# Kernel tuning notes

Measured on AMD Instinct MI355X. Metric: run time of the kernel, lower is better.

Reference implementation:

```python
import jax, jax.numpy as jnp
import numpy as np

B, S, LC, DIM, H, FFN = 1, 3600, 512, 1536, 12, 8960
HD = DIM // H          # 128
GRID = (4, 30, 30)     # f*h*w == S
K_LEN = 9900           # hardcoded k_lens in SelfAttention.forward
EPS = 1e-6

def _rope_axis_angles(n_pos, dim):
    inv = 1.0 / np.power(10000.0, np.arange(0, dim, 2, dtype=np.float64) / dim)
    return np.outer(np.arange(n_pos), inv)

def _build_rope(grid, head_dim):
    c = head_dim // 2                      # 64
    c1, c2 = c - 2 * (c // 3), c // 3      # 22, 21 (Wan 3D rope split)
    f, h, w = grid
    af = _rope_axis_angles(f, 2 * c1)
    ah = _rope_axis_angles(h, 2 * c2)
    aw = _rope_axis_angles(w, 2 * c2)
    ang = np.concatenate([
        np.broadcast_to(af[:, None, None, :], (f, h, w, c1)),
        np.broadcast_to(ah[None, :, None, :], (f, h, w, c2)),
        np.broadcast_to(aw[None, None, :, :], (f, h, w, c2)),
    ], axis=-1).reshape(f * h * w, c)
    return np.cos(ang).astype(np.float32), np.sin(ang).astype(np.float32)

def setup_inputs():
    key = jax.random.key(0)
    ks = iter(jax.random.split(key, 40))
    cos, sin = _build_rope(GRID, HD)
    inp = {
        'x': jax.random.normal(next(ks), (B, S, DIM), dtype=jnp.float32),
        'context': jax.random.normal(next(ks), (B, LC, DIM), dtype=jnp.float32),
        't_mod': 0.1 * jax.random.normal(next(ks), (B, 6, DIM), dtype=jnp.float32),
        'rope_cos': jnp.asarray(cos), 'rope_sin': jnp.asarray(sin),
        'modulation': jax.random.normal(next(ks), (1, 6, DIM), dtype=jnp.float32) / DIM ** 0.5,
    }
    for p in ('sa', 'ca'):
        for w in ('q', 'k', 'v', 'o'):
            inp[p + '_' + w + 'w'] = 0.02 * jax.random.normal(next(ks), (DIM, DIM), dtype=jnp.float32)
            inp[p + '_' + w + 'b'] = jnp.zeros((DIM,), jnp.float32)
        inp[p + '_nq'] = jnp.ones((DIM,), jnp.float32)
        inp[p + '_nk'] = jnp.ones((DIM,), jnp.float32)
    inp['n3_w'] = jnp.ones((DIM,), jnp.float32)
    inp['n3_b'] = jnp.zeros((DIM,), jnp.float32)
    inp['ffn_w1'] = 0.02 * jax.random.normal(next(ks), (DIM, FFN), dtype=jnp.float32)
    inp['ffn_b1'] = jnp.zeros((FFN,), jnp.float32)
    inp['ffn_w2'] = 0.02 * jax.random.normal(next(ks), (FFN, DIM), dtype=jnp.float32)
    inp['ffn_b2'] = jnp.zeros((DIM,), jnp.float32)
    return inp

def _rms(x, w):
    x32 = x.astype(jnp.float32)
    n = x32 * jax.lax.rsqrt(jnp.mean(x32 * x32, axis=-1, keepdims=True) + EPS)
    return n.astype(x.dtype) * w

def _ln(x, w=None, b=None):
    mu = jnp.mean(x, axis=-1, keepdims=True)
    var = jnp.mean(jnp.square(x - mu), axis=-1, keepdims=True)
    y = (x - mu) * jax.lax.rsqrt(var + EPS)
    return y if w is None else y * w + b

def _rope(x, cos, sin):
    b, s, h, d = x.shape
    x2 = x.reshape(b, s, h, d // 2, 2)
    xe, xo = x2[..., 0], x2[..., 1]
    c, sn = cos[None, :, None, :], sin[None, :, None, :]
    return jnp.stack([xe * c - xo * sn, xe * sn + xo * c], axis=-1).reshape(b, s, h, d)

def _attn(q, k, v, k_len=None):
    # q,k,v: [B,S,H,D]
    scores = jnp.einsum('bqhd,bkhd->bhqk', q, k) * (q.shape[-1] ** -0.5)
    if k_len is not None:
        mask = jnp.arange(k.shape[1]) < k_len
        scores = jnp.where(mask[None, None, None, :], scores, jnp.finfo(scores.dtype).min)
    return jnp.einsum('bhqk,bkhd->bqhd', jax.nn.softmax(scores, axis=-1), v)

def reference(x, context, t_mod, rope_cos, rope_sin, modulation,
              sa_qw, sa_qb, sa_kw, sa_kb, sa_vw, sa_vb, sa_ow, sa_ob, sa_nq, sa_nk,
              ca_qw, ca_qb, ca_kw, ca_kb, ca_vw, ca_vb, ca_ow, ca_ob, ca_nq, ca_nk,
              n3_w, n3_b, ffn_w1, ffn_b1, ffn_w2, ffn_b2):
    mod = modulation + t_mod                      # [B,6,DIM]
    sh_msa, sc_msa, g_msa, sh_mlp, sc_mlp, g_mlp = [mod[:, i:i + 1] for i in range(6)]
    b = x.shape[0]
    # --- self-attention with AdaLN modulate + 3D RoPE + k_lens mask ---
    h = _ln(x) * (1 + sc_msa) + sh_msa
    q = _rms(h @ sa_qw + sa_qb, sa_nq).reshape(b, -1, H, HD)
    k = _rms(h @ sa_kw + sa_kb, sa_nk).reshape(b, -1, H, HD)
    v = (h @ sa_vw + sa_vb).reshape(b, -1, H, HD)
    a = _attn(_rope(q, rope_cos, rope_sin), _rope(k, rope_cos, rope_sin), v, k_len=K_LEN)
    x = x + g_msa * (a.reshape(b, -1, DIM) @ sa_ow + sa_ob)
    # --- cross-attention ---
    hc = _ln(x, n3_w, n3_b)
    q = _rms(hc @ ca_qw + ca_qb, ca_nq).reshape(b, -1, H, HD)
    k = _rms(context @ ca_kw + ca_kb, ca_nk).reshape(b, -1, H, HD)
    v = (context @ ca_vw + ca_vb).reshape(b, -1, H, HD)
    x = x + (_attn(q, k, v).reshape(b, -1, DIM) @ ca_ow + ca_ob)
    # --- gated FFN with AdaLN modulate ---
    h = _ln(x) * (1 + sc_mlp) + sh_mlp
    h = jax.nn.gelu(h @ ffn_w1 + ffn_b1, approximate=True) @ ffn_w2 + ffn_b2
    return x + g_mlp * h
```

## Files before the change

### kernel.cpp

```cpp
#include <hip/hip_runtime.h>
#include <cstdint>

#define S_LEN 3600
#define DMODEL 1536
#define LCTX 512
#define NH 12
#define HDIM 128
#define FFND 8960
#define SPAD_SELF 3648

typedef short v8s __attribute__((ext_vector_type(8)));
typedef float v4f __attribute__((ext_vector_type(4)));
typedef unsigned short u16b;
typedef unsigned int u32b;

#define AS1 __attribute__((address_space(1)))
#define AS3 __attribute__((address_space(3)))

__device__ __forceinline__ void gl_lds16(const void* g, void* l){
  __builtin_amdgcn_global_load_lds((AS1 const void*)g, (AS3 void*)l, 16, 0, 0);
}

__device__ __forceinline__ u16b f2b(float f){
  union { float f; u32b i; } x; x.f = f;
  u32b r = x.i + 0x7fffu + ((x.i >> 16) & 1u);
  return (u16b)(r >> 16);
}

__device__ __forceinline__ u32b cvtpk(float a, float b){
  u32b r;
  asm("v_cvt_pk_bf16_f32 %0, %1, %2" : "=v"(r) : "v"(a), "v"(b));
  return r;
}

__device__ __forceinline__ int swz4(int row){ return (row ^ (row >> 2)) & 3; }

__device__ __forceinline__ int xcd_swz(int orig, int nwg){
  int q8 = nwg >> 3, r8 = nwg & 7;
  int xcd = orig & 7, idx = orig >> 3;
  return (xcd < r8 ? xcd * (q8 + 1) : r8 * (q8 + 1) + (xcd - r8) * q8) + idx;
}

__global__ void add_vec(const float* __restrict__ a, const float* __restrict__ b,
                        float* __restrict__ o, int n){
  int i = blockIdx.x * 256 + threadIdx.x;
  if (i < n) o[i] = a[i] + b[i];
}

__global__ void f2b_kernel(const float* __restrict__ in, u16b* __restrict__ out, int n){
  int i = blockIdx.x * 256 + threadIdx.x;
  if (i < n) out[i] = f2b(in[i]);
}

struct WJob { const float* W; u16b* WT; int K; int N; int t0; };
struct WJobs { WJob j[10]; };

__global__ __launch_bounds__(256) void wconv(WJobs jobs){
  __shared__ float tile[32][33];
  int b = blockIdx.x;
  int ji = 0;
  #pragma unroll
  for (int i = 0; i < 10; ++i) if (b >= jobs.j[i].t0) ji = i;
  WJob jb = jobs.j[ji];
  int rel = b - jb.t0;
  int ntn = jb.N / 32;
  int k0 = (rel / ntn) * 32, n0 = (rel % ntn) * 32;
  int tx = threadIdx.x & 31, ty = threadIdx.x >> 5;
  #pragma unroll
  for (int r = ty; r < 32; r += 8) tile[r][tx] = jb.W[(size_t)(k0 + r) * jb.N + n0 + tx];
  __syncthreads();
  #pragma unroll
  for (int r = ty; r < 32; r += 8) jb.WT[(size_t)(n0 + r) * jb.K + k0 + tx] = f2b(tile[tx][r]);
}

__global__ __launch_bounds__(256) void vtrans(const u16b* __restrict__ V,
                                              u16b* __restrict__ Vt,
                                              int S, int Spad){
  __shared__ u16b t[32][136];
  int h = blockIdx.y, kb = blockIdx.x * 32, tid = threadIdx.x;
  int row = tid >> 3, ch = tid & 7;
  int key = kb + row;
  if (key < S){
    float4 a = *(const float4*)(V + (size_t)key * DMODEL + h * HDIM + ch * 16);
    float4 b = *(const float4*)(V + (size_t)key * DMODEL + h * HDIM + ch * 16 + 8);
    *(float4*)&t[row][ch * 16] = a;
    *(float4*)&t[row][ch * 16 + 8] = b;
  } else {
    float4 z = {0.f, 0.f, 0.f, 0.f};
    *(float4*)&t[row][ch * 16] = z;
    *(float4*)&t[row][ch * 16 + 8] = z;
  }
  __syncthreads();
  int hd = tid >> 1, kc = (tid & 1) * 16;
  u16b* dst = Vt + ((size_t)h * HDIM + hd) * Spad + kb + kc;
  #pragma unroll
  for (int e = 0; e < 16; e += 2){
    u32b pk = ((u32b)t[kc + e][hd]) | (((u32b)t[kc + e + 1][hd]) << 16);
    *(u32b*)(dst + e) = pk;
  }
}

__global__ __launch_bounds__(256) void ln_mod(const float* __restrict__ X,
                                              const float* __restrict__ gamma,
                                              const float* __restrict__ beta,
                                              float gadd, u16b* __restrict__ out){
  int row = blockIdx.x;
  const float* xr = X + (size_t)row * DMODEL;
  int tid = threadIdx.x;
  float v[6]; float s1 = 0.f, s2 = 0.f;
  #pragma unroll
  for (int j = 0; j < 6; ++j){ v[j] = xr[tid + j * 256]; s1 += v[j]; s2 += v[j] * v[j]; }
  #pragma unroll
  for (int o = 1; o < 64; o <<= 1){ s1 += __shfl_xor(s1, o); s2 += __shfl_xor(s2, o); }
  __shared__ float red[8];
  int wid = tid >> 6, lane = tid & 63;
  if (!lane){ red[wid * 2] = s1; red[wid * 2 + 1] = s2; }
  __syncthreads();
  s1 = red[0] + red[2] + red[4] + red[6];
  s2 = red[1] + red[3] + red[5] + red[7];
  float mu = s1 / DMODEL;
  float var = s2 / DMODEL - mu * mu;
  float rstd = rsqrtf(var + 1e-6f);
  #pragma unroll
  for (int j = 0; j < 6; ++j){
    int c = tid + j * 256;
    float g = gamma[c] + gadd;
    float b = beta[c];
    out[(size_t)row * DMODEL + c] = f2b((v[j] - mu) * rstd * g + b);
  }
}

__global__ __launch_bounds__(256) void rms_rope(const float* __restrict__ X,
                                                const float* __restrict__ w,
                                                const float* __restrict__ cosT,
                                                const float* __restrict__ sinT,
                                                float qmul,
                                                u16b* __restrict__ out){
  int row = blockIdx.x;
  const float* xr = X + (size_t)row * DMODEL;
  int tid = threadIdx.x;
  float2 v[3]; float ss = 0.f;
  #pragma unroll
  for (int j = 0; j < 3; ++j){
    v[j] = *(const float2*)(xr + 2 * (tid + j * 256));
    ss += v[j].x * v[j].x + v[j].y * v[j].y;
  }
  #pragma unroll
  for (int o = 1; o < 64; o <<= 1) ss += __shfl_xor(ss, o);
  __shared__ float red[4];
  int wid = tid >> 6, lane = tid & 63;
  if (!lane) red[wid] = ss;
  __syncthreads();
  ss = red[0] + red[1] + red[2] + red[3];
  float rstd = rsqrtf(ss / DMODEL + 1e-6f);
  #pragma unroll
  for (int j = 0; j < 3; ++j){
    int p = tid + j * 256;
    float xe = v[j].x * rstd * w[2 * p];
    float xo = v[j].y * rstd * w[2 * p + 1];
    float oe, oo;
    if (cosT){
      int d = p & 63;
      float c = cosT[row * 64 + d], sn = sinT[row * 64 + d];
      oe = xe * c - xo * sn; oo = xe * sn + xo * c;
    } else { oe = xe; oo = xo; }
    oe *= qmul; oo *= qmul;
    u32b packed = ((u32b)f2b(oe)) | (((u32b)f2b(oo)) << 16);
    *(u32b*)(out + (size_t)row * DMODEL + 2 * p) = packed;
  }
}

struct Seg { const float* bias; float* outF; u16b* outB; };
struct Segs { Seg s[3]; };

template<int EPI>
__global__ __launch_bounds__(256, 2) void gemm_bt(
    const u16b* __restrict__ A, const u16b* __restrict__ BT,
    const float* __restrict__ bias, float* __restrict__ outF,
    float* __restrict__ outF2, u16b* __restrict__ outB,
    int M, int N, int K, int kLen)
{
  __shared__ char Ls[3][16384];
  const int tid = threadIdx.x, lane = tid & 63, wid = tid >> 6;
  const int nwg = gridDim.x * gridDim.y;
  const int swz = xcd_swz(blockIdx.x + gridDim.x * blockIdx.y, nwg);
  const int bm = (swz % gridDim.x) * 128, bn = (swz / gridDim.x) * 128;
  const int kbase = blockIdx.z * kLen;
  const int wm = (wid >> 1) * 64, wn = (wid & 1) * 64;
  v4f acc[4][4] = {};

  const u16b* pA[2]; const u16b* pB[2];
  #pragma unroll
  for (int c = 0; c < 2; ++c){
    int row = c * 64 + (tid >> 2);
    int col = (tid & 3) ^ swz4(row);
    pA[c] = A + (size_t)min(bm + row, M - 1) * K + kbase + col * 8;
    pB[c] = BT + (size_t)(bn + row) * K + kbase + col * 8;
  }
  auto stage = [&](int b){
    char* Lb = Ls[b];
    #pragma unroll
    for (int c = 0; c < 2; ++c){
      gl_lds16(pA[c], Lb + (c * 256 + tid) * 16);
      gl_lds16(pB[c], Lb + 8192 + (c * 256 + tid) * 16);
      pA[c] += 32; pB[c] += 32;
    }
  };

  const int chk = lane >> 4, qr = lane & 15;
  int offA[4], offB[4];
  #pragma unroll
  for (int f = 0; f < 4; ++f){
    int ra = wm + f * 16 + qr;
    offA[f] = ra * 64 + ((chk ^ swz4(ra)) * 16);
    int rb = wn + f * 16 + qr;
    offB[f] = 8192 + rb * 64 + ((chk ^ swz4(rb)) * 16);
  }

  const int nt = kLen / 32;
  stage(0); stage(1);
  int s = 0, sp = 2;
  for (int t = 0; t < nt; ++t){
    if (t + 1 < nt) asm volatile("s_waitcnt vmcnt(4)" ::: "memory");
    else            asm volatile("s_waitcnt vmcnt(0)" ::: "memory");
    __builtin_amdgcn_s_barrier();
    if (t + 2 < nt) stage(sp);
    char* Lb = Ls[s];
    v8s af[4], bfr[4];
    #pragma unroll
    for (int f = 0; f < 4; ++f){
      af[f] = *(const v8s*)(Lb + offA[f]);
      bfr[f] = *(const v8s*)(Lb + offB[f]);
    }
    __builtin_amdgcn_s_setprio(1);
    #pragma unroll
    for (int i = 0; i < 4; ++i)
      #pragma unroll
      for (int j = 0; j < 4; ++j)
        acc[i][j] = __builtin_amdgcn_mfma_f32_16x16x32_bf16(af[i], bfr[j], acc[i][j], 0, 0, 0);
    __builtin_amdgcn_s_setprio(0);
    s = (s == 2) ? 0 : s + 1;
    sp = (sp == 2) ? 0 : sp + 1;
  }
  const int rr = lane >> 4;
  float* op6 = (EPI == 6) ? (blockIdx.z ? outF2 : outF) : outF;
  #pragma unroll
  for (int i = 0; i < 4; ++i){
    #pragma unroll
    for (int j = 0; j < 4; ++j){
      int n = bn + wn + j * 16 + qr;
      float bv = (EPI == 3) ? bias[n] : 0.f;
      #pragma unroll
      for (int r = 0; r < 4; ++r){
        int m = bm + wm + i * 16 + rr * 4 + r;
        if (m < M){
          float val = acc[i][j][r] + bv;
          size_t idx = (size_t)m * N + n;
          if (EPI == 3){
            float t3 = val * val * val;
            float g = val / (1.f + __expf(-1.5957691216057308f * (val + 0.044715f * t3)));
            outB[idx] = f2b(g);
          } else if (EPI == 5){
            outF[(size_t)blockIdx.z * M * N + idx] = val;
          } else {
            op6[idx] = val;
          }
        }
      }
    }
  }
}

__global__ __launch_bounds__(256, 2) void gemm_seg(
    const u16b* __restrict__ A, const u16b* __restrict__ BT,
    Segs segs, int M, int N, int K)
{
  __shared__ char Ls[3][16384];
  const int tid = threadIdx.x, lane = tid & 63, wid = tid >> 6;
  const int nwg = gridDim.x * gridDim.y;
  const int swz = xcd_swz(blockIdx.x + gridDim.x * blockIdx.y, nwg);
  const int bm = (swz % gridDim.x) * 128, bn = (swz / gridDim.x) * 128;
  const int wm = (wid >> 1) * 64, wn = (wid & 1) * 64;
  v4f acc[4][4] = {};

  const u16b* pA[2]; const u16b* pB[2];
  #pragma unroll
  for (int c = 0; c < 2; ++c){
    int row = c * 64 + (tid >> 2);
    int col = (tid & 3) ^ swz4(row);
    pA[c] = A + (size_t)min(bm + row, M - 1) * K + col * 8;
    pB[c] = BT + (size_t)(bn + row) * K + col * 8;
  }
  auto stage = [&](int b){
    char* Lb = Ls[b];
    #pragma unroll
    for (int c = 0; c < 2; ++c){
      gl_lds16(pA[c], Lb + (c * 256 + tid) * 16);
      gl_lds16(pB[c], Lb + 8192 + (c * 256 + tid) * 16);
      pA[c] += 32; pB[c] += 32;
    }
  };

  const int chk = lane >> 4, qr = lane & 15;
  int offA[4], offB[4];
  #pragma unroll
  for (int f = 0; f < 4; ++f){
    int ra = wm + f * 16 + qr;
    offA[f] = ra * 64 + ((chk ^ swz4(ra)) * 16);
    int rb = wn + f * 16 + qr;
    offB[f] = 8192 + rb * 64 + ((chk ^ swz4(rb)) * 16);
  }

  const int nt = K / 32;
  stage(0); stage(1);
  int s = 0, sp = 2;
  for (int t = 0; t < nt; ++t){
    if (t + 1 < nt) asm volatile("s_waitcnt vmcnt(4)" ::: "memory");
    else            asm volatile("s_waitcnt vmcnt(0)" ::: "memory");
    __builtin_amdgcn_s_barrier();
    if (t + 2 < nt) stage(sp);
    char* Lb = Ls[s];
    v8s af[4], bfr[4];
    #pragma unroll
    for (int f = 0; f < 4; ++f){
      af[f] = *(const v8s*)(Lb + offA[f]);
      bfr[f] = *(const v8s*)(Lb + offB[f]);
    }
    __builtin_amdgcn_s_setprio(1);
    #pragma unroll
    for (int i = 0; i < 4; ++i)
      #pragma unroll
      for (int j = 0; j < 4; ++j)
        acc[i][j] = __builtin_amdgcn_mfma_f32_16x16x32_bf16(af[i], bfr[j], acc[i][j], 0, 0, 0);
    __builtin_amdgcn_s_setprio(0);
    s = (s == 2) ? 0 : s + 1;
    sp = (sp == 2) ? 0 : sp + 1;
  }
  const int seg = bn / 1536;
  const Seg sg = segs.s[seg];
  const int rr = lane >> 4;
  #pragma unroll
  for (int i = 0; i < 4; ++i){
    #pragma unroll
    for (int j = 0; j < 4; ++j){
      int nloc = bn - seg * 1536 + wn + j * 16 + qr;
      float bv = sg.bias[nloc];
      #pragma unroll
      for (int r = 0; r < 4; ++r){
        int m = bm + wm + i * 16 + rr * 4 + r;
        if (m < M){
          float val = acc[i][j][r] + bv;
          size_t idx = (size_t)m * 1536 + nloc;
          if (sg.outB) sg.outB[idx] = f2b(val);
          else sg.outF[idx] = val;
        }
      }
    }
  }
}

__global__ __launch_bounds__(256) void red2(const float* __restrict__ p0,
                                            const float* __restrict__ p1,
                                            const float* __restrict__ res,
                                            const float* __restrict__ gate,
                                            const float* __restrict__ bias,
                                            float* __restrict__ out, int total){
  int i4 = blockIdx.x * 256 + threadIdx.x;
  if (i4 * 4 >= total) return;
  int base = i4 * 4, n = base % DMODEL;
  float4 a = *(const float4*)(p0 + base);
  float4 b = *(const float4*)(p1 + base);
  float4 bv = *(const float4*)(bias + n);
  float gx = 1.f, gy = 1.f, gz = 1.f, gw = 1.f;
  if (gate){ float4 g = *(const float4*)(gate + n); gx = g.x; gy = g.y; gz = g.z; gw = g.w; }
  float rx = 0.f, ry = 0.f, rz = 0.f, rw = 0.f;
  if (res){ float4 r = *(const float4*)(res + base); rx = r.x; ry = r.y; rz = r.z; rw = r.w; }
  float4 o;
  o.x = rx + gx * (a.x + b.x + bv.x);
  o.y = ry + gy * (a.y + b.y + bv.y);
  o.z = rz + gz * (a.z + b.z + bv.z);
  o.w = rw + gw * (a.w + b.w + bv.w);
  *(float4*)(out + base) = o;
}

__global__ __launch_bounds__(256) void ffn2_reduce(const float* __restrict__ part,
                                                   const float* __restrict__ res,
                                                   const float* __restrict__ bias,
                                                   const float* __restrict__ gate,
                                                   float* __restrict__ out, int total){
  int i4 = blockIdx.x * 256 + threadIdx.x;
  if (i4 * 4 >= total) return;
  int base = i4 * 4;
  int n = base % DMODEL;
  float4 p0 = *(const float4*)(part + base);
  float4 p1 = *(const float4*)(part + (size_t)total + base);
  float4 p2 = *(const float4*)(part + 2 * (size_t)total + base);
  float4 p3 = *(const float4*)(part + 3 * (size_t)total + base);
  float4 rs = *(const float4*)(res + base);
  float4 bv = *(const float4*)(bias + n);
  float4 gv = *(const float4*)(gate + n);
  float4 o;
  o.x = rs.x + gv.x * (p0.x + p1.x + p2.x + p3.x + bv.x);
  o.y = rs.y + gv.y * (p0.y + p1.y + p2.y + p3.y + bv.y);
  o.z = rs.z + gv.z * (p0.z + p1.z + p2.z + p3.z + bv.z);
  o.w = rs.w + gv.w * (p0.w + p1.w + p2.w + p3.w + bv.w);
  *(float4*)(out + base) = o;
}

__global__ __launch_bounds__(256) void merge_o(const float* __restrict__ op0,
                                               const float* __restrict__ op1,
                                               const float2* __restrict__ ml,
                                               u16b* __restrict__ outO, int Sq){
  int i4 = blockIdx.x * 256 + threadIdx.x;
  const int perRow = DMODEL / 4;
  if (i4 >= Sq * perRow) return;
  int row = i4 / perRow, c4 = (i4 % perRow) * 4;
  int h = c4 >> 7;
  float2 ml0 = ml[h * Sq + row];
  float2 ml1 = ml[NH * Sq + h * Sq + row];
  float M = fmaxf(ml0.x, ml1.x);
  float w0 = exp2f(ml0.x - M), w1 = exp2f(ml1.x - M);
  float inv = 1.f / (ml0.y * w0 + ml1.y * w1);
  float4 a = *(const float4*)(op0 + (size_t)row * DMODEL + c4);
  float4 b = *(const float4*)(op1 + (size_t)row * DMODEL + c4);
  u32b lo = ((u32b)f2b((a.x * w0 + b.x * w1) * inv)) | (((u32b)f2b((a.y * w0 + b.y * w1) * inv)) << 16);
  u32b hi = ((u32b)f2b((a.z * w0 + b.z * w1) * inv)) | (((u32b)f2b((a.w * w0 + b.w * w1) * inv)) << 16);
  uint2 w2; w2.x = lo; w2.y = hi;
  *(uint2*)(outO + (size_t)row * DMODEL + c4) = w2;
}

__global__ __launch_bounds__(256, 4) void flash_attn(
    const u16b* __restrict__ Q, const u16b* __restrict__ Kp,
    const u16b* __restrict__ Vt, u16b* __restrict__ O,
    float* __restrict__ op0, float* __restrict__ op1,
    float2* __restrict__ mlbuf,
    int Sq, int Sk, int ksplit, int Spad)
{
  __shared__ char KV[32768];
  __shared__ char Pall[8192];
  const int tid = threadIdx.x, lane = tid & 63, wid = tid >> 6;
  const int h = blockIdx.y;
  const int z = blockIdx.z;
  const int kbeg = z * ksplit;
  const int kend = min(kbeg + ksplit, Sk);
  const int q0 = blockIdx.x * 64 + wid * 16;
  const int qq = lane & 15, cc = lane >> 4;
  char* Kb = KV; char* Vb = KV + 16384;
  char* Pb = Pall + wid * 2048;

  v8s qf[4];
  {
    int qrow = min(q0 + qq, Sq - 1);
    const u16b* qp = Q + (size_t)qrow * DMODEL + h * HDIM + cc * 8;
    #pragma unroll
    for (int ks = 0; ks < 4; ++ks) qf[ks] = *(const v8s*)(qp + ks * 32);
  }

  auto stage = [&](int kb0){
    #pragma unroll
    for (int c = 0; c < 4; ++c){
      int seg = wid * 4 + c;
      int g = seg * 64 + lane;
      int krow = g >> 4, kcol = (g & 15) ^ (krow & 7);
      gl_lds16(Kp + (size_t)min(kb0 + krow, Sk - 1) * DMODEL + h * HDIM + kcol * 8,
               Kb + seg * 1024);
      int vrow = g >> 3, vcol = (g & 7) ^ (vrow & 7);
      gl_lds16(Vt + ((size_t)h * HDIM + vrow) * Spad + kb0 + vcol * 8,
               Vb + seg * 1024);
    }
  };

  float mrun = -1e30f, lrun = 0.f;
  v4f oacc[8] = {};
  const int nt = (kend - kbeg + 63) >> 6;

  for (int t = 0; t < nt; ++t){
    int kb0 = kbeg + (t << 6);
    stage(kb0);
    __syncthreads();
    v4f sc[4];
    __builtin_amdgcn_s_setprio(1);
    #pragma unroll
    for (int sub = 0; sub < 4; ++sub){
      v4f sa = {0.f, 0.f, 0.f, 0.f};
      int row = sub * 16 + qq;
      #pragma unroll
      for (int ks = 0; ks < 4; ++ks){
        v8s kf = *(const v8s*)(Kb + row * 256 + (((ks * 4 + cc) ^ (row & 7)) * 16));
        sa = __builtin_amdgcn_mfma_f32_16x16x32_bf16(kf, qf[ks], sa, 0, 0, 0);
      }
      sc[sub] = sa;
    }
    __builtin_amdgcn_s_setprio(0);
    if (kb0 + 64 > kend){
      #pragma unroll
      for (int sub = 0; sub < 4; ++sub)
        #pragma unroll
        for (int r = 0; r < 4; ++r)
          if (kb0 + sub * 16 + cc * 4 + r >= kend) sc[sub][r] = -1e30f;
    }
    float m01 = fmaxf(fmaxf(sc[0][0], sc[0][1]), fmaxf(sc[0][2], sc[0][3]));
    float m23 = fmaxf(fmaxf(sc[1][0], sc[1][1]), fmaxf(sc[1][2], sc[1][3]));
    float m45 = fmaxf(fmaxf(sc[2][0], sc[2][1]), fmaxf(sc[2][2], sc[2][3]));
    float m67 = fmaxf(fmaxf(sc[3][0], sc[3][1]), fmaxf(sc[3][2], sc[3][3]));
    float pmax = fmaxf(fmaxf(m01, m23), fmaxf(m45, m67));
    pmax = fmaxf(pmax, __shfl_xor(pmax, 16));
    pmax = fmaxf(pmax, __shfl_xor(pmax, 32));
    if (!__all(pmax <= mrun + 11.54f)){
      float mnew = fmaxf(mrun, pmax);
      float alpha = exp2f(mrun - mnew);
      mrun = mnew;
      float alr[4];
      #pragma unroll
      for (int r = 0; r < 4; ++r) alr[r] = __shfl(alpha, cc * 4 + r);
      #pragma unroll
      for (int f = 0; f < 8; ++f)
        #pragma unroll
        for (int r = 0; r < 4; ++r) oacc[f][r] *= alr[r];
      lrun *= alpha;
    }
    float csum = 0.f;
    #pragma unroll
    for (int sub = 0; sub < 4; ++sub){
      float s0 = 0.f, s1 = 0.f;
      #pragma unroll
      for (int r = 0; r < 4; r += 2){
        float p0 = exp2f(sc[sub][r] - mrun);
        float p1 = exp2f(sc[sub][r + 1] - mrun);
        sc[sub][r] = p0; sc[sub][r + 1] = p1;
        s0 += p0; s1 += p1;
      }
      csum += s0 + s1;
    }
    csum += __shfl_xor(csum, 16);
    csum += __shfl_xor(csum, 32);
    lrun += csum;
    #pragma unroll
    for (int sub = 0; sub < 4; ++sub){
      uint2 w2;
      w2.x = cvtpk(sc[sub][0], sc[sub][1]);
      w2.y = cvtpk(sc[sub][2], sc[sub][3]);
      int gI = sub * 2 + (cc >> 1);
      *(uint2*)(Pb + qq * 128 + ((gI ^ (qq & 7)) * 16) + (cc & 1) * 8) = w2;
    }
    v8s pf0 = *(const v8s*)(Pb + qq * 128 + (((cc) ^ (qq & 7)) * 16));
    v8s pf1 = *(const v8s*)(Pb + qq * 128 + (((4 + cc) ^ (qq & 7)) * 16));
    __builtin_amdgcn_s_setprio(1);
    #pragma unroll
    for (int hdb = 0; hdb < 8; ++hdb){
      int row = hdb * 16 + qq;
      v8s vf0 = *(const v8s*)(Vb + row * 128 + (((cc) ^ (row & 7)) * 16));
      v8s vf1 = *(const v8s*)(Vb + row * 128 + (((4 + cc) ^ (row & 7)) * 16));
      oacc[hdb] = __builtin_amdgcn_mfma_f32_16x16x32_bf16(pf0, vf0, oacc[hdb], 0, 0, 0);
      oacc[hdb] = __builtin_amdgcn_mfma_f32_16x16x32_bf16(pf1, vf1, oacc[hdb], 0, 0, 0);
    }
    __builtin_amdgcn_s_setprio(0);
    __syncthreads();
  }

  if (mlbuf){
    float* op = z ? op1 : op0;
    #pragma unroll
    for (int hdb = 0; hdb < 8; ++hdb)
      #pragma unroll
      for (int r = 0; r < 4; ++r){
        int qrow = q0 + cc * 4 + r;
        if (qrow < Sq)
          op[(size_t)qrow * DMODEL + h * HDIM + hdb * 16 + qq] = oacc[hdb][r];
      }
    if (cc == 0 && q0 + qq < Sq)
      mlbuf[(size_t)z * NH * Sq + (size_t)h * Sq + q0 + qq] = make_float2(mrun, lrun);
  } else {
    float linv = 1.f / lrun;
    float lr[4];
    #pragma unroll
    for (int r = 0; r < 4; ++r) lr[r] = __shfl(linv, cc * 4 + r);
    #pragma unroll
    for (int hdb = 0; hdb < 8; ++hdb)
      #pragma unroll
      for (int r = 0; r < 4; ++r){
        int qrow = q0 + cc * 4 + r;
        if (qrow < Sq)
          O[(size_t)qrow * DMODEL + h * HDIM + hdb * 16 + qq] = f2b(oacc[hdb][r] * lr[r]);
      }
  }
}

extern "C" void kernel_launch(void* const* d_in, const int* in_sizes, int n_in,
                              void* d_out, int out_size, void* d_ws, size_t ws_size,
                              hipStream_t stream){
  (void)in_sizes; (void)n_in; (void)out_size; (void)ws_size;
  const float* x     = (const float*)d_in[0];
  const float* ctx   = (const float*)d_in[1];
  const float* t_mod = (const float*)d_in[2];
  const float* ropec = (const float*)d_in[3];
  const float* ropes = (const float*)d_in[4];
  const float* modu  = (const float*)d_in[5];
  const float* sa_qw = (const float*)d_in[6];  const float* sa_qb = (const float*)d_in[7];
  const float* sa_kw = (const float*)d_in[8];  const float* sa_kb = (const float*)d_in[9];
  const float* sa_vw = (const float*)d_in[10]; const float* sa_vb = (const float*)d_in[11];
  const float* sa_ow = (const float*)d_in[12]; const float* sa_ob = (const float*)d_in[13];
  const float* sa_nq = (const float*)d_in[14]; const float* sa_nk = (const float*)d_in[15];
  const float* ca_qw = (const float*)d_in[16]; const float* ca_qb = (const float*)d_in[17];
  const float* ca_kw = (const float*)d_in[18]; const float* ca_kb = (const float*)d_in[19];
  const float* ca_vw = (const float*)d_in[20]; const float* ca_vb = (const float*)d_in[21];
  const float* ca_ow = (const float*)d_in[22]; const float* ca_ob = (const float*)d_in[23];
  const float* ca_nq = (const float*)d_in[24]; const float* ca_nk = (const float*)d_in[25];
  const float* n3w   = (const float*)d_in[26]; const float* n3b   = (const float*)d_in[27];
  const float* fw1   = (const float*)d_in[28]; const float* fb1   = (const float*)d_in[29];
  const float* fw2   = (const float*)d_in[30]; const float* fb2   = (const float*)d_in[31];
  float* out = (float*)d_out;

  const float QSCALE = 0.08838834764831845f * 1.4426950408889634f;

  char* wsp = (char*)d_ws;
  size_t off = 0;
  auto alloc = [&](size_t b){ void* p = wsp + off; off += (b + 255) & ~(size_t)255; return p; };
  const size_t WW = (size_t)DMODEL * DMODEL * 2;
  float* modc = (float*)alloc(6 * DMODEL * 4);
  u16b* w1T   = (u16b*)alloc((size_t)FFND * DMODEL * 2);
  u16b* w2T   = (u16b*)alloc((size_t)DMODEL * FFND * 2);
  u16b* h_bf  = (u16b*)alloc((size_t)S_LEN * DMODEL * 2);
  float* pre0 = (float*)alloc((size_t)S_LEN * DMODEL * 4);
  size_t region0 = off;
  u16b* sa_qkvT = (u16b*)alloc(3 * WW);
  u16b* sa_owT  = (u16b*)alloc(WW);
  u16b* ca_qwT  = (u16b*)alloc(WW);
  u16b* ca_kvT  = (u16b*)alloc(2 * WW);
  u16b* ca_owT  = (u16b*)alloc(WW);
  float* x2    = (float*)alloc((size_t)S_LEN * DMODEL * 4);
  float* pre2  = (float*)alloc((size_t)LCTX * DMODEL * 4);
  u16b* qb     = (u16b*)alloc((size_t)S_LEN * DMODEL * 2);
  u16b* kb     = (u16b*)alloc((size_t)S_LEN * DMODEL * 2);
  u16b* vb     = (u16b*)alloc((size_t)S_LEN * DMODEL * 2);
  u16b* ab     = (u16b*)alloc((size_t)S_LEN * DMODEL * 2);
  u16b* ctxb   = (u16b*)alloc((size_t)LCTX * DMODEL * 2);
  u16b* k2b    = (u16b*)alloc((size_t)LCTX * DMODEL * 2);
  u16b* v2b    = (u16b*)alloc((size_t)LCTX * DMODEL * 2);
  u16b* vts    = (u16b*)alloc((size_t)NH * HDIM * SPAD_SELF * 2);
  u16b* vtc    = (u16b*)alloc((size_t)NH * HDIM * LCTX * 2);
  u16b* fmid = (u16b*)(wsp + region0);
  float* fpart = (float*)(wsp + region0 + (size_t)S_LEN * FFND * 2);

  add_vec<<<36, 256, 0, stream>>>(modu, t_mod, modc, 6 * DMODEL);

  WJobs jobs; int t = 0;
  auto addjob = [&](int i, const float* w_, u16b* wt, int K, int N){
    jobs.j[i].W = w_; jobs.j[i].WT = wt; jobs.j[i].K = K; jobs.j[i].N = N; jobs.j[i].t0 = t;
    t += (K / 32) * (N / 32);
  };
  addjob(0, sa_qw, sa_qkvT, DMODEL, DMODEL);
  addjob(1, sa_kw, sa_qkvT + (size_t)DMODEL * DMODEL, DMODEL, DMODEL);
  addjob(2, sa_vw, sa_qkvT + (size_t)2 * DMODEL * DMODEL, DMODEL, DMODEL);
  addjob(3, sa_ow, sa_owT, DMODEL, DMODEL);
  addjob(4, ca_qw, ca_qwT, DMODEL, DMODEL);
  addjob(5, ca_kw, ca_kvT, DMODEL, DMODEL);
  addjob(6, ca_vw, ca_kvT + (size_t)DMODEL * DMODEL, DMODEL, DMODEL);
  addjob(7, ca_ow, ca_owT, DMODEL, DMODEL);
  addjob(8, fw1, w1T, DMODEL, FFND);
  addjob(9, fw2, w2T, FFND, DMODEL);
  wconv<<<t, 256, 0, stream>>>(jobs);

  f2b_kernel<<<(LCTX * DMODEL) / 256, 256, 0, stream>>>(ctx, ctxb, LCTX * DMODEL);

  const int RED_G = (S_LEN * DMODEL / 4 + 255) / 256;

  ln_mod<<<S_LEN, 256, 0, stream>>>(x, modc + DMODEL, modc, 1.f, h_bf);
  {
    Segs sg;
    sg.s[0] = { sa_qb, pre0, nullptr };
    sg.s[1] = { sa_kb, x2,   nullptr };
    sg.s[2] = { sa_vb, nullptr, vb   };
    gemm_seg<<<dim3(29, 36), 256, 0, stream>>>(h_bf, sa_qkvT, sg, S_LEN, 3 * DMODEL, DMODEL);
  }
  rms_rope<<<S_LEN, 256, 0, stream>>>(pre0, sa_nq, ropec, ropes, QSCALE, qb);
  rms_rope<<<S_LEN, 256, 0, stream>>>(x2, sa_nk, ropec, ropes, 1.f, kb);
  vtrans<<<dim3(SPAD_SELF / 32, 12), 256, 0, stream>>>(vb, vts, S_LEN, SPAD_SELF);
  flash_attn<<<dim3(57, 12, 2), 256, 0, stream>>>(qb, kb, vts, ab,
      (float*)pre0, (float*)x2, (float2*)vb, S_LEN, S_LEN, 1856, SPAD_SELF);
  merge_o<<<RED_G, 256, 0, stream>>>(
      (const float*)pre0, (const float*)x2, (const float2*)vb, ab, S_LEN);
  gemm_bt<6><<<dim3(29, 12, 2), 256, 0, stream>>>(ab, sa_owT, nullptr,
      (float*)pre0, (float*)qb, nullptr, S_LEN, DMODEL, DMODEL, 768);
  red2<<<RED_G, 256, 0, stream>>>((const float*)pre0, (const float*)qb,
      x, modc + 2 * DMODEL, sa_ob, x2, S_LEN * DMODEL);

  ln_mod<<<S_LEN, 256, 0, stream>>>(x2, n3w, n3b, 0.f, h_bf);
  gemm_bt<6><<<dim3(29, 12, 2), 256, 0, stream>>>(h_bf, ca_qwT, nullptr,
      (float*)qb, (float*)vb, nullptr, S_LEN, DMODEL, DMODEL, 768);
  red2<<<RED_G, 256, 0, stream>>>((const float*)qb, (const float*)vb,
      nullptr, nullptr, ca_qb, pre0, S_LEN * DMODEL);
  {
    Segs sg;
    sg.s[0] = { ca_kb, pre2, nullptr };
    sg.s[1] = { ca_vb, nullptr, v2b  };
    sg.s[2] = { ca_vb, nullptr, v2b  };
    gemm_seg<<<dim3(4, 24), 256, 0, stream>>>(ctxb, ca_kvT, sg, LCTX, 2 * DMODEL, DMODEL);
  }
  rms_rope<<<S_LEN, 256, 0, stream>>>(pre0, ca_nq, nullptr, nullptr, QSCALE, qb);
  rms_rope<<<LCTX, 256, 0, stream>>>(pre2, ca_nk, nullptr, nullptr, 1.f, k2b);
  vtrans<<<dim3(16, 12), 256, 0, stream>>>(v2b, vtc, LCTX, LCTX);
  flash_attn<<<dim3(57, 12, 2), 256, 0, stream>>>(qb, k2b, vtc, ab,
      (float*)pre0, (float*)kb, (float2*)vts, S_LEN, LCTX, 256, LCTX);
  merge_o<<<RED_G, 256, 0, stream>>>(
      (const float*)pre0, (const float*)kb, (const float2*)vts, ab, S_LEN);
  gemm_bt<6><<<dim3(29, 12, 2), 256, 0, stream>>>(ab, ca_owT, nullptr,
      (float*)qb, (float*)sa_qkvT, nullptr, S_LEN, DMODEL, DMODEL, 768);
  red2<<<RED_G, 256, 0, stream>>>((const float*)qb, (const float*)sa_qkvT,
      x2, nullptr, ca_ob, pre0, S_LEN * DMODEL);

  ln_mod<<<S_LEN, 256, 0, stream>>>(pre0, modc + 4 * DMODEL, modc + 3 * DMODEL, 1.f, h_bf);
  gemm_bt<3><<<dim3(29, 70), 256, 0, stream>>>(h_bf, w1T, fb1,
      nullptr, nullptr, fmid, S_LEN, FFND, DMODEL, DMODEL);
  gemm_bt<5><<<dim3(29, 12, 4), 256, 0, stream>>>(fmid, w2T, nullptr,
      fpart, nullptr, nullptr, S_LEN, DMODEL, FFND, FFND / 4);
  ffn2_reduce<<<RED_G, 256, 0, stream>>>(fpart, pre0, fb2, modc + 5 * DMODEL, out, S_LEN * DMODEL);
}
```

Before: 949.2 us.

## Fuse residual reduce with layernorm, widen flash-attn blocks, halve FFN2 split-K

Adds a red2_ln kernel that sums the split-K partials, bias, gate and residual, then applies layernorm in one pass. This replaces two separate red2+ln_mod launches and removes an extra read of the fp32 residual stream. Flash attention now uses 512-thread blocks covering 128 query rows, so each staged K/V tile is shared by twice as many queries; this raises LDS use per block and changes the occupancy hint. FFN2 split-K drops from 4 to 2, which halves partial-buffer traffic but leaves fewer blocks for the GEMM.

```diff
diff --git a/kernel.cpp b/kernel.cpp
--- a/kernel.cpp
+++ b/kernel.cpp
@@ -124,9 +124,44 @@
   #pragma unroll
   for (int j = 0; j < 6; ++j){
     int c = tid + j * 256;
-    float g = gamma[c] + gadd;
-    float b = beta[c];
-    out[(size_t)row * DMODEL + c] = f2b((v[j] - mu) * rstd * g + b);
+    out[(size_t)row * DMODEL + c] = f2b((v[j] - mu) * rstd * (gamma[c] + gadd) + beta[c]);
+  }
+}
+
+__global__ __launch_bounds__(256) void red2_ln(
+    const float* __restrict__ p0, const float* __restrict__ p1,
+    const float* __restrict__ res, const float* __restrict__ gate,
+    const float* __restrict__ bias,
+    const float* __restrict__ gamma, const float* __restrict__ beta, float gadd,
+    float* __restrict__ yOut, u16b* __restrict__ hOut)
+{
+  int row = blockIdx.x, tid = threadIdx.x;
+  size_t base = (size_t)row * DMODEL;
+  float y[6]; float s1 = 0.f, s2 = 0.f;
+  #pragma unroll
+  for (int j = 0; j < 6; ++j){
+    int c = tid + j * 256;
+    float v = p0[base + c] + p1[base + c] + bias[c];
+    if (gate) v *= gate[c];
+    v += res[base + c];
+    y[j] = v; s1 += v; s2 += v * v;
+  }
+  #pragma unroll
+  for (int o = 1; o < 64; o <<= 1){ s1 += __shfl_xor(s1, o); s2 += __shfl_xor(s2, o); }
+  __shared__ float red[8];
+  int wid = tid >> 6, lane = tid & 63;
+  if (!lane){ red[wid * 2] = s1; red[wid * 2 + 1] = s2; }
+  __syncthreads();
+  s1 = red[0] + red[2] + red[4] + red[6];
+  s2 = red[1] + red[3] + red[5] + red[7];
+  float mu = s1 / DMODEL;
+  float var = s2 / DMODEL - mu * mu;
+  float rstd = rsqrtf(var + 1e-6f);
+  #pragma unroll
+  for (int j = 0; j < 6; ++j){
+    int c = tid + j * 256;
+    yOut[base + c] = y[j];
+    hOut[base + c] = f2b((y[j] - mu) * rstd * (gamma[c] + gadd) + beta[c]);
   }
 }
 
@@ -383,30 +418,6 @@
   *(float4*)(out + base) = o;
 }
 
-__global__ __launch_bounds__(256) void ffn2_reduce(const float* __restrict__ part,
-                                                   const float* __restrict__ res,
-                                                   const float* __restrict__ bias,
-                                                   const float* __restrict__ gate,
-                                                   float* __restrict__ out, int total){
-  int i4 = blockIdx.x * 256 + threadIdx.x;
-  if (i4 * 4 >= total) return;
-  int base = i4 * 4;
-  int n = base % DMODEL;
-  float4 p0 = *(const float4*)(part + base);
-  float4 p1 = *(const float4*)(part + (size_t)total + base);
-  float4 p2 = *(const float4*)(part + 2 * (size_t)total + base);
-  float4 p3 = *(const float4*)(part + 3 * (size_t)total + base);
-  float4 rs = *(const float4*)(res + base);
-  float4 bv = *(const float4*)(bias + n);
-  float4 gv = *(const float4*)(gate + n);
-  float4 o;
-  o.x = rs.x + gv.x * (p0.x + p1.x + p2.x + p3.x + bv.x);
-  o.y = rs.y + gv.y * (p0.y + p1.y + p2.y + p3.y + bv.y);
-  o.z = rs.z + gv.z * (p0.z + p1.z + p2.z + p3.z + bv.z);
-  o.w = rs.w + gv.w * (p0.w + p1.w + p2.w + p3.w + bv.w);
-  *(float4*)(out + base) = o;
-}
-
 __global__ __launch_bounds__(256) void merge_o(const float* __restrict__ op0,
                                                const float* __restrict__ op1,
                                                const float2* __restrict__ ml,
@@ -429,7 +440,7 @@
   *(uint2*)(outO + (size_t)row * DMODEL + c4) = w2;
 }
 
-__global__ __launch_bounds__(256, 4) void flash_attn(
+__global__ __launch_bounds__(512, 6) void flash_attn(
     const u16b* __restrict__ Q, const u16b* __restrict__ Kp,
     const u16b* __restrict__ Vt, u16b* __restrict__ O,
     float* __restrict__ op0, float* __restrict__ op1,
@@ -437,13 +448,13 @@
     int Sq, int Sk, int ksplit, int Spad)
 {
   __shared__ char KV[32768];
-  __shared__ char Pall[8192];
+  __shared__ char Pall[16384];
   const int tid = threadIdx.x, lane = tid & 63, wid = tid >> 6;
   const int h = blockIdx.y;
   const int z = blockIdx.z;
   const int kbeg = z * ksplit;
   const int kend = min(kbeg + ksplit, Sk);
-  const int q0 = blockIdx.x * 64 + wid * 16;
+  const int q0 = blockIdx.x * 128 + wid * 16;
   const int qq = lane & 15, cc = lane >> 4;
   char* Kb = KV; char* Vb = KV + 16384;
   char* Pb = Pall + wid * 2048;
@@ -458,15 +469,14 @@
 
   auto stage = [&](int kb0){
     #pragma unroll
-    for (int c = 0; c < 4; ++c){
-      int seg = wid * 4 + c;
-      int g = seg * 64 + lane;
-      int krow = g >> 4, kcol = (g & 15) ^ (krow & 7);
+    for (int c = 0; c < 2; ++c){
+      int l = c * 512 + tid;
+      int krow = l >> 4, kcol = (l & 15) ^ (krow & 7);
       gl_lds16(Kp + (size_t)min(kb0 + krow, Sk - 1) * DMODEL + h * HDIM + kcol * 8,
-               Kb + seg * 1024);
-      int vrow = g >> 3, vcol = (g & 7) ^ (vrow & 7);
+               Kb + l * 16);
+      int vrow = l >> 3, vcol = (l & 7) ^ (vrow & 7);
       gl_lds16(Vt + ((size_t)h * HDIM + vrow) * Spad + kb0 + vcol * 8,
-               Vb + seg * 1024);
+               Vb + l * 16);
     }
   };
 
@@ -676,16 +686,15 @@
   rms_rope<<<S_LEN, 256, 0, stream>>>(pre0, sa_nq, ropec, ropes, QSCALE, qb);
   rms_rope<<<S_LEN, 256, 0, stream>>>(x2, sa_nk, ropec, ropes, 1.f, kb);
   vtrans<<<dim3(SPAD_SELF / 32, 12), 256, 0, stream>>>(vb, vts, S_LEN, SPAD_SELF);
-  flash_attn<<<dim3(57, 12, 2), 256, 0, stream>>>(qb, kb, vts, ab,
+  flash_attn<<<dim3(29, 12, 2), 512, 0, stream>>>(qb, kb, vts, ab,
       (float*)pre0, (float*)x2, (float2*)vb, S_LEN, S_LEN, 1856, SPAD_SELF);
   merge_o<<<RED_G, 256, 0, stream>>>(
       (const float*)pre0, (const float*)x2, (const float2*)vb, ab, S_LEN);
   gemm_bt<6><<<dim3(29, 12, 2), 256, 0, stream>>>(ab, sa_owT, nullptr,
       (float*)pre0, (float*)qb, nullptr, S_LEN, DMODEL, DMODEL, 768);
-  red2<<<RED_G, 256, 0, stream>>>((const float*)pre0, (const float*)qb,
-      x, modc + 2 * DMODEL, sa_ob, x2, S_LEN * DMODEL);
-
-  ln_mod<<<S_LEN, 256, 0, stream>>>(x2, n3w, n3b, 0.f, h_bf);
+  red2_ln<<<S_LEN, 256, 0, stream>>>((const float*)pre0, (const float*)qb,
+      x, modc + 2 * DMODEL, sa_ob, n3w, n3b, 0.f, x2, h_bf);
+
   gemm_bt<6><<<dim3(29, 12, 2), 256, 0, stream>>>(h_bf, ca_qwT, nullptr,
       (float*)qb, (float*)vb, nullptr, S_LEN, DMODEL, DMODEL, 768);
   red2<<<RED_G, 256, 0, stream>>>((const float*)qb, (const float*)vb,
@@ -700,19 +709,19 @@
   rms_rope<<<S_LEN, 256, 0, stream>>>(pre0, ca_nq, nullptr, nullptr, QSCALE, qb);
   rms_rope<<<LCTX, 256, 0, stream>>>(pre2, ca_nk, nullptr, nullptr, 1.f, k2b);
   vtrans<<<dim3(16, 12), 256, 0, stream>>>(v2b, vtc, LCTX, LCTX);
-  flash_attn<<<dim3(57, 12, 2), 256, 0, stream>>>(qb, k2b, vtc, ab,
+  flash_attn<<<dim3(29, 12, 2), 512, 0, stream>>>(qb, k2b, vtc, ab,
       (float*)pre0, (float*)kb, (float2*)vts, S_LEN, LCTX, 256, LCTX);
   merge_o<<<RED_G, 256, 0, stream>>>(
       (const float*)pre0, (const float*)kb, (const float2*)vts, ab, S_LEN);
   gemm_bt<6><<<dim3(29, 12, 2), 256, 0, stream>>>(ab, ca_owT, nullptr,
       (float*)qb, (float*)sa_qkvT, nullptr, S_LEN, DMODEL, DMODEL, 768);
-  red2<<<RED_G, 256, 0, stream>>>((const float*)qb, (const float*)sa_qkvT,
-      x2, nullptr, ca_ob, pre0, S_LEN * DMODEL);
-
-  ln_mod<<<S_LEN, 256, 0, stream>>>(pre0, modc + 4 * DMODEL, modc + 3 * DMODEL, 1.f, h_bf);
+  red2_ln<<<S_LEN, 256, 0, stream>>>((const float*)qb, (const float*)sa_qkvT,
+      x2, nullptr, ca_ob, modc + 4 * DMODEL, modc + 3 * DMODEL, 1.f, pre0, h_bf);
+
   gemm_bt<3><<<dim3(29, 70), 256, 0, stream>>>(h_bf, w1T, fb1,
       nullptr, nullptr, fmid, S_LEN, FFND, DMODEL, DMODEL);
-  gemm_bt<5><<<dim3(29, 12, 4), 256, 0, stream>>>(fmid, w2T, nullptr,
-      fpart, nullptr, nullptr, S_LEN, DMODEL, FFND, FFND / 4);
-  ffn2_reduce<<<RED_G, 256, 0, stream>>>(fpart, pre0, fb2, modc + 5 * DMODEL, out, S_LEN * DMODEL);
-}
+  gemm_bt<5><<<dim3(29, 12, 2), 256, 0, stream>>>(fmid, w2T, nullptr,
+      fpart, nullptr, nullptr, S_LEN, DMODEL, FFND, FFND / 2);
+  red2<<<RED_G, 256, 0, stream>>>(fpart, fpart + (size_t)S_LEN * DMODEL,
+      pre0, modc + 5 * DMODEL, fb2, out, S_LEN * DMODEL);
+}
```

New measurement: 1.204 ms. +26.9%, slower.
